# Performance work log

Measured on AMD Instinct MI355X. Metric: run time of the kernel, lower is better.

## Reference

```python
import jax, jax.numpy as jnp
import numpy as np

NF, NS, GP = 5, 27, 4


def conv2d(x, w, b):
    y = jax.lax.conv_general_dilated(x, w, (1, 1), 'SAME',
                                     dimension_numbers=('NCHW', 'OIHW', 'NCHW'))
    return y + b[None, :, None, None]


def trilinear_sample(frames, tc, yc, xc):
    # frames: [b, nf, h, w]; tc/yc/xc: [b, NS, h, w] absolute (t, y, x) coords
    b, nf, h, w = frames.shape
    tc = jnp.clip(tc, 0.0, nf - 1.0)
    yc = jnp.clip(yc, 0.0, h - 1.0)
    xc = jnp.clip(xc, 0.0, w - 1.0)
    t0 = jnp.floor(tc); y0 = jnp.floor(yc); x0 = jnp.floor(xc)
    wt = tc - t0; wy = yc - y0; wx = xc - x0
    t0i = t0.astype(jnp.int32); y0i = y0.astype(jnp.int32); x0i = x0.astype(jnp.int32)
    t1i = jnp.minimum(t0i + 1, nf - 1)
    y1i = jnp.minimum(y0i + 1, h - 1)
    x1i = jnp.minimum(x0i + 1, w - 1)
    flat = frames.reshape(b, -1)

    def g(ti, yi, xi):
        idx = (ti * h + yi) * w + xi  # [b, NS, h, w]
        return jnp.take_along_axis(flat, idx.reshape(b, -1), axis=1).reshape(idx.shape)

    c000 = g(t0i, y0i, x0i); c001 = g(t0i, y0i, x1i)
    c010 = g(t0i, y1i, x0i); c011 = g(t0i, y1i, x1i)
    c100 = g(t1i, y0i, x0i); c101 = g(t1i, y0i, x1i)
    c110 = g(t1i, y1i, x0i); c111 = g(t1i, y1i, x1i)
    c00 = c000 * (1 - wx) + c001 * wx
    c01 = c010 * (1 - wx) + c011 * wx
    c10 = c100 * (1 - wx) + c101 * wx
    c11 = c110 * (1 - wx) + c111 * wx
    c0 = c00 * (1 - wy) + c01 * wy
    c1 = c10 * (1 - wy) + c11 * wy
    return c0 * (1 - wt) + c1 * wt


def samp(frames, offset):
    # offset: [b, NS*3, h, w] -> per-sample (dt, dy, dx)
    b, nf, h, w = frames.shape
    off = offset.reshape(b, NS, 3, h, w)
    grid = np.stack(np.meshgrid(np.arange(-1, 2), np.arange(-1, 2), np.arange(-1, 2),
                                indexing='ij'), -1).reshape(NS, 3).astype(np.float32)
    bt = jnp.asarray(grid[:, 0] + (NF - 1) // 2)[None, :, None, None]
    by = jnp.asarray(grid[:, 1])[None, :, None, None]
    bx = jnp.asarray(grid[:, 2])[None, :, None, None]
    yy = jnp.arange(h, dtype=frames.dtype)[None, None, :, None]
    xx = jnp.arange(w, dtype=frames.dtype)[None, None, None, :]
    tc = off[:, :, 0] + bt
    yc = off[:, :, 1] + by + yy
    xc = off[:, :, 2] + bx + xx
    return trilinear_sample(frames, tc, yc, xc)  # [b, NS, h, w]


def reference(frames, ow1, ob1, ow2, ob2, ow3, ob3, ww1, wb1, ww2, wb2, ww3, wb3):
    b, c, h, w = frames.shape
    # OffsetNet: two relu convs -> feat (128 ch), head -> offsets (NS*3 ch)
    f1 = jax.nn.relu(conv2d(frames, ow1, ob1))
    feat = jax.nn.relu(conv2d(f1, ow2, ob2))
    offset = conv2d(feat, ow3, ob3)
    samples = samp(frames, offset)  # [b, 27, h, w]
    cat = jnp.concatenate([frames, feat, samples], axis=1)  # [b, 160, h, w]
    # WeightsNet: three conv+relu
    wgt = jax.nn.relu(conv2d(cat, ww1, wb1))
    wgt = jax.nn.relu(conv2d(wgt, ww2, wb2))
    wgt = jax.nn.relu(conv2d(wgt, ww3, wb3))  # [b, 27, h, w]
    npg = NS // GP  # 6 -> only first GP*npg=24 samples used (torch.split + range(gp))
    s = samples[:, :GP * npg].reshape(b, GP, npg, h, w)
    wg = wgt[:, :GP * npg].reshape(b, GP, npg, h, w)
    gp_pred = GP * jnp.sum(s * wg, axis=2)  # [b, 4, h, w]
    avg = jnp.sum(gp_pred, axis=1, keepdims=True) / NS
    return gp_pred, avg


def setup_inputs() -> dict:
    key = jax.random.key(0)
    ks = jax.random.split(key, 8)
    B, H, W = 4, 512, 512

    def he(k, shape):
        fan_in = shape[1] * shape[2] * shape[3]
        return jax.random.normal(k, shape, jnp.float32) * np.sqrt(2.0 / fan_in)

    return {
        'frames': jax.random.uniform(ks[0], (B, NF, H, W), jnp.float32),
        'ow1': he(ks[1], (64, NF, 3, 3)), 'ob1': jnp.zeros((64,), jnp.float32),
        'ow2': he(ks[2], (128, 64, 3, 3)), 'ob2': jnp.zeros((128,), jnp.float32),
        'ow3': he(ks[3], (NS * 3, 128, 3, 3)) * 0.1, 'ob3': jnp.zeros((NS * 3,), jnp.float32),
        'ww1': he(ks[4], (64, NF + 128 + NS, 3, 3)), 'wb1': jnp.zeros((64,), jnp.float32),
        'ww2': he(ks[5], (64, 64, 3, 3)), 'wb2': jnp.zeros((64,), jnp.float32),
        'ww3': he(ks[6], (NS, 64, 3, 3)), 'wb3': jnp.zeros((NS,), jnp.float32),
    }
```

## Files before the change

kernel.cpp:

```cpp
#include <hip/hip_runtime.h>

#define HH 512
#define WW 512
#define HWP (HH * WW)

typedef unsigned short bf16_t;
typedef short bf16x8 __attribute__((ext_vector_type(8)));
typedef float f32x4 __attribute__((ext_vector_type(4)));
typedef unsigned short us4 __attribute__((ext_vector_type(4)));
typedef unsigned short us8 __attribute__((ext_vector_type(8)));

__device__ __forceinline__ float bf2f(bf16_t h) {
    union { unsigned int u; float f; } v; v.u = ((unsigned int)h) << 16; return v.f;
}
__device__ __forceinline__ bf16_t f2bf(float f) {
    union { float f; unsigned int u; } v; v.f = f;
    unsigned int r = (v.u + 0x7FFFu + ((v.u >> 16) & 1u)) >> 16;
    return (bf16_t)r;
}
__device__ __forceinline__ bf16x8 as_bf(us8 v) {
    union { us8 a; bf16x8 b; } u; u.a = v; return u.b;
}
__device__ __forceinline__ void gload16(const void* g, void* l) {
    __builtin_amdgcn_global_load_lds(
        (const __attribute__((address_space(1))) void*)g,
        (__attribute__((address_space(3))) void*)l, 16, 0, 0);
}

__global__ __launch_bounds__(256) void wprep_all(
    const float* __restrict__ w1, const float* __restrict__ w2,
    const float* __restrict__ w3, const float* __restrict__ w4,
    const float* __restrict__ w5, const float* __restrict__ w6,
    bf16_t* __restrict__ dst)
{
    int i = blockIdx.x * 256 + threadIdx.x;
    if (i >= 350720) return;
    if (i >= 350208) { dst[i] = 0; return; }
    const float* w; int Cout, Cin, COTF, KS, perm, base;
    if (i < 18432)       { w = w1; base = 0;      Cout = 64;  Cin = 5;   COTF = 4; KS = 1; perm = 0; }
    else if (i < 92160)  { w = w2; base = 18432;  Cout = 128; Cin = 64;  COTF = 8; KS = 2; perm = 0; }
    else if (i < 202752) { w = w3; base = 92160;  Cout = 81;  Cin = 128; COTF = 6; KS = 4; perm = 0; }
    else if (i < 294912) { w = w4; base = 202752; Cout = 64;  Cin = 160; COTF = 4; KS = 5; perm = 1; }
    else if (i < 331776) { w = w5; base = 294912; Cout = 64;  Cin = 64;  COTF = 4; KS = 2; perm = 0; }
    else                 { w = w6; base = 331776; Cout = 27;  Cin = 64;  COTF = 2; KS = 2; perm = 0; }
    int r = i - base;
    int j = r & 7;
    int lane = (r >> 3) & 63;
    int cot = (r >> 9) % COTF;
    int rest = r / (512 * COTF);
    int ks = rest % KS, tap = rest / KS;
    int col = lane & 15, hi = lane >> 4;
    int co = cot * 16 + col;
    int ci = ks * 32 + hi * 8 + j;
    float v = 0.f;
    if (co < Cout && ci < Cin) {
        int rci = ci;
        if (perm) rci = (ci < 128) ? ci + 5 : (ci < 133 ? ci - 128 : ci);
        v = w[((size_t)co * Cin + rci) * 9 + tap];
    }
    dst[i] = f2bf(v);
}

template<int COT, int KS>
__global__ __launch_bounds__(256, 2) void tconv(
    const bf16_t* __restrict__ in, size_t inImgStride,
    const bf16_t* __restrict__ wt, const float* __restrict__ bias,
    bf16_t* __restrict__ out, size_t outImgStride,
    int COTF, int Cout, int relu, const bf16_t* __restrict__ zp)
{
    __shared__ us8 buf[2][1584];
    const int tid = threadIdx.x;
    const int wave = tid >> 6, lane = tid & 63;
    const int col = lane & 15, hi = lane >> 4;
    const int img = blockIdx.y >> 7;
    const int yb0 = (blockIdx.y & 127) * 4;
    const int xb = blockIdx.x * 64;
    const int czbase = blockIdx.z * COT;
    const size_t slab = (size_t)HH * WW * 32;

    in += (size_t)img * inImgStride;
    out += (size_t)img * outImgStride;

    int gofs[7];
    bool ok[7];
#pragma unroll
    for (int k = 0; k < 7; ++k) {
        int u = tid + k * 256;
        if (u >= 1584) u = 1583;
        int row = (unsigned)u / 264u;
        int rem = u - row * 264;
        int px = rem >> 2, cs = rem & 3;
        int c = (cs - (px >> 1)) & 3;
        int yin = yb0 - 1 + row;
        int gx = xb - 1 + px;
        ok[k] = ((unsigned)yin < (unsigned)HH) && ((unsigned)gx < (unsigned)WW);
        gofs[k] = ok[k] ? (int)(((size_t)yin * WW + gx) * 32 + c * 8) : 0;
    }

    auto STAGE = [&](int nb, int ks) {
#pragma unroll
        for (int k = 0; k < 7; ++k) {
            if (k == 6 && tid >= 48) continue;
            const bf16_t* g = ok[k] ? in + (size_t)ks * slab + gofs[k] : zp;
            gload16(g, (void*)&buf[nb][k * 256 + wave * 64]);
        }
    };

    f32x4 acc[4][COT] = {};
    bf16x8 a[9][COT];

    auto ALOAD = [&](int ks) {
#pragma unroll
        for (int t = 0; t < 9; ++t) {
#pragma unroll
            for (int c = 0; c < COT; ++c)
                a[t][c] = *(const bf16x8*)(wt
                    + (((size_t)t * KS + ks) * COTF + czbase + c) * 512 + lane * 8);
        }
    };

    auto COMPUTE = [&](int cb) {
#pragma unroll
        for (int dy = 0; dy < 3; ++dy) {
#pragma unroll
            for (int dx = 0; dx < 3; ++dx) {
                bf16x8 b[4];
#pragma unroll
                for (int pt = 0; pt < 4; ++pt) {
                    int X = pt * 16 + col + dx;
                    int unit = (wave + dy) * 264 + X * 4 + ((hi + (X >> 1)) & 3);
                    b[pt] = as_bf(buf[cb][unit]);
                }
#pragma unroll
                for (int c = 0; c < COT; ++c) {
#pragma unroll
                    for (int pt = 0; pt < 4; ++pt)
                        acc[pt][c] = __builtin_amdgcn_mfma_f32_16x16x32_bf16(
                            a[dy * 3 + dx][c], b[pt], acc[pt][c], 0, 0, 0);
                }
            }
        }
    };

    STAGE(0, 0);
    for (int ks = 0; ks < KS; ++ks) {
        ALOAD(ks);
        __builtin_amdgcn_sched_barrier(0);
        if (ks + 1 < KS) {
            STAGE((ks + 1) & 1, ks + 1);
            __builtin_amdgcn_sched_barrier(0);
            asm volatile("s_waitcnt vmcnt(7)" ::: "memory");
        } else {
            asm volatile("s_waitcnt vmcnt(0)" ::: "memory");
        }
        __builtin_amdgcn_sched_barrier(0);
        __builtin_amdgcn_s_barrier();
        __builtin_amdgcn_sched_barrier(0);
        COMPUTE(ks & 1);
        __builtin_amdgcn_s_barrier();
        __builtin_amdgcn_sched_barrier(0);
    }

    int y = yb0 + wave;
#pragma unroll
    for (int c = 0; c < COT; ++c) {
        int chbase = (czbase + c) * 16 + hi * 4;
        int slice = chbase >> 5, rem = chbase & 31;
        float bv[4];
#pragma unroll
        for (int j = 0; j < 4; ++j) {
            int co = chbase + j;
            bv[j] = (co < Cout) ? bias[co] : 0.f;
        }
#pragma unroll
        for (int pt = 0; pt < 4; ++pt) {
            int x = xb + pt * 16 + col;
            us4 o;
#pragma unroll
            for (int j = 0; j < 4; ++j) {
                float v = acc[pt][c][j] + bv[j];
                if (relu) v = fmaxf(v, 0.f);
                o[j] = f2bf(v);
            }
            *(us4*)(out + (((size_t)slice * HH + y) * WW + x) * 32 + rem) = o;
        }
    }
}

__global__ __launch_bounds__(256) void tr_fr32(
    const float* __restrict__ fr0, int img0,
    bf16_t* __restrict__ dst0, size_t stride)
{
    int img = blockIdx.y;
    int i = blockIdx.x * 256 + threadIdx.x;
    const float* fr = fr0 + (size_t)(img0 + img) * 5 * HWP;
    bf16_t* dst = dst0 + (size_t)img * stride;
    us8 v0 = {};
#pragma unroll
    for (int c = 0; c < 5; ++c) v0[c] = f2bf(fr[(size_t)c * HWP + i]);
    us8 z = {};
    us8* o = (us8*)(dst + (size_t)i * 32);
    o[0] = v0; o[1] = z; o[2] = z; o[3] = z;
}

__global__ __launch_bounds__(256, 4) void sample27f(
    const float* __restrict__ fr0, int img0,
    const bf16_t* __restrict__ of0, size_t stride,
    bf16_t* __restrict__ cat0)
{
    int img = blockIdx.y;
    int i = blockIdx.x * 256 + threadIdx.x;
    int y = i >> 9, x = i & 511;
    const float* f = fr0 + (size_t)(img0 + img) * 5 * HWP;
    const bf16_t* off = of0 + (size_t)img * stride;
    bf16_t* cat = cat0 + (size_t)img * stride;

    us8 ov[12];
#pragma unroll
    for (int sl = 0; sl < 3; ++sl)
#pragma unroll
        for (int c = 0; c < 4; ++c)
            ov[sl * 4 + c] = *(const us8*)(off
                + (((size_t)sl * HH + y) * WW + x) * 32 + c * 8);

    us8 outv[4];
#pragma unroll
    for (int c = 0; c < 5; ++c)
        outv[0][c] = f2bf(f[(size_t)c * HWP + i]);

#pragma unroll
    for (int s = 0; s < 27; ++s) {
        float dt  = bf2f((bf16_t)ov[(3 * s) >> 3][(3 * s) & 7]);
        float dyo = bf2f((bf16_t)ov[(3 * s + 1) >> 3][(3 * s + 1) & 7]);
        float dxo = bf2f((bf16_t)ov[(3 * s + 2) >> 3][(3 * s + 2) & 7]);
        float tc = dt + (float)(s / 9 + 1);
        float yc = dyo + (float)((s / 3) % 3 - 1) + (float)y;
        float xc = dxo + (float)(s % 3 - 1) + (float)x;
        tc = fminf(fmaxf(tc, 0.f), 4.f);
        yc = fminf(fmaxf(yc, 0.f), 511.f);
        xc = fminf(fmaxf(xc, 0.f), 511.f);
        float t0f = floorf(tc), y0f = floorf(yc), x0f = floorf(xc);
        float wt = tc - t0f, wy = yc - y0f, wx = xc - x0f;
        int t0 = (int)t0f, y0 = (int)y0f, x0 = (int)x0f;
        int t1 = min(t0 + 1, 4), y1 = min(y0 + 1, 511), x1 = min(x0 + 1, 511);
        float c000 = f[((size_t)t0 * HH + y0) * WW + x0];
        float c001 = f[((size_t)t0 * HH + y0) * WW + x1];
        float c010 = f[((size_t)t0 * HH + y1) * WW + x0];
        float c011 = f[((size_t)t0 * HH + y1) * WW + x1];
        float c100 = f[((size_t)t1 * HH + y0) * WW + x0];
        float c101 = f[((size_t)t1 * HH + y0) * WW + x1];
        float c110 = f[((size_t)t1 * HH + y1) * WW + x0];
        float c111 = f[((size_t)t1 * HH + y1) * WW + x1];
        float c00 = c000 * (1.f - wx) + c001 * wx;
        float c01 = c010 * (1.f - wx) + c011 * wx;
        float c10 = c100 * (1.f - wx) + c101 * wx;
        float c11 = c110 * (1.f - wx) + c111 * wx;
        float c0 = c00 * (1.f - wy) + c01 * wy;
        float c1 = c10 * (1.f - wy) + c11 * wy;
        int ch = 5 + s;
        outv[ch >> 3][ch & 7] = f2bf(c0 * (1.f - wt) + c1 * wt);
    }

    us8* o = (us8*)(cat + ((size_t)y * WW + x) * 32);
    o[0] = outv[0]; o[1] = outv[1]; o[2] = outv[2]; o[3] = outv[3];
}

__global__ __launch_bounds__(256) void combineN(
    const bf16_t* __restrict__ cat0, const bf16_t* __restrict__ wg0,
    size_t stride, float* __restrict__ out, int img0)
{
    int img = blockIdx.y;
    int i = blockIdx.x * 256 + threadIdx.x;
    int gimg = img0 + img;
    const bf16_t* sp = cat0 + (size_t)img * stride + (size_t)i * 32 + 5;
    const bf16_t* wp = wg0 + (size_t)img * stride + (size_t)i * 32;
    float* ogp  = out + (size_t)gimg * 4 * HWP;
    float* oavg = out + (size_t)16 * HWP + (size_t)gimg * HWP;
    float total = 0.f;
#pragma unroll
    for (int g = 0; g < 4; ++g) {
        float acc = 0.f;
#pragma unroll
        for (int j = 0; j < 6; ++j)
            acc += bf2f(sp[g * 6 + j]) * bf2f(wp[g * 6 + j]);
        float gp = 4.f * acc;
        ogp[(size_t)g * HWP + i] = gp;
        total += gp;
    }
    oavg[i] = total / 27.f;
}

static inline int cdiv(int a, int b) { return (a + b - 1) / b; }

extern "C" void kernel_launch(void* const* d_in, const int* in_sizes, int n_in,
                              void* d_out, int out_size, void* d_ws, size_t ws_size,
                              hipStream_t stream)
{
    const float* frames = (const float*)d_in[0];
    const float* ow1 = (const float*)d_in[1];
    const float* ob1 = (const float*)d_in[2];
    const float* ow2 = (const float*)d_in[3];
    const float* ob2 = (const float*)d_in[4];
    const float* ow3 = (const float*)d_in[5];
    const float* ob3 = (const float*)d_in[6];
    const float* ww1 = (const float*)d_in[7];
    const float* wb1 = (const float*)d_in[8];
    const float* ww2 = (const float*)d_in[9];
    const float* wb2 = (const float*)d_in[10];
    const float* ww3 = (const float*)d_in[11];
    const float* wb3 = (const float*)d_in[12];
    float* out = (float*)d_out;

    bf16_t* Wp = (bf16_t*)d_ws;
    const size_t wo1 = 0;
    const size_t wo2 = 18432;
    const size_t wo3 = 92160;
    const size_t wo4 = 202752;
    const size_t wo5 = 294912;
    const size_t wo6 = 331776;
    const size_t wzp = 350208;
    const size_t wtot = 350720;

    const size_t SLAB = (size_t)HH * WW * 32;
    const size_t PerImg = 7 * SLAB;

    size_t availElems = ws_size / sizeof(bf16_t);
    int NB = 1;
    if (wtot + 4 * PerImg <= availElems) NB = 4;
    else if (wtot + 2 * PerImg <= availElems) NB = 2;

    bf16_t* ZP = Wp + wzp;
    bf16_t* WS = Wp + wtot;

    wprep_all<<<cdiv(350720, 256), 256, 0, stream>>>(ow1, ow2, ow3, ww1, ww2, ww3, Wp);

    for (int s = 0; s < 4; s += NB) {
        int nb = (4 - s < NB) ? (4 - s) : NB;
        bf16_t* S0 = WS;
        bf16_t* S2 = WS + 2 * SLAB;
        bf16_t* S4 = WS + 4 * SLAB;
        bf16_t* S5 = WS + 5 * SLAB;
        bf16_t* S6 = WS + 6 * SLAB;

        tr_fr32<<<dim3(1024, nb), 256, 0, stream>>>(frames, s, S6, PerImg);
        tconv<4, 1><<<dim3(8, 128 * nb, 1), 256, 0, stream>>>(
            S6, PerImg, Wp + wo1, ob1, S4, PerImg, 4, 64, 1, ZP);
        tconv<4, 2><<<dim3(8, 128 * nb, 2), 256, 0, stream>>>(
            S4, PerImg, Wp + wo2, ob2, S0, PerImg, 8, 128, 1, ZP);
        tconv<3, 4><<<dim3(8, 128 * nb, 2), 256, 0, stream>>>(
            S0, PerImg, Wp + wo3, ob3, S4, PerImg, 6, 81, 0, ZP);
        sample27f<<<dim3(1024, nb), 256, 0, stream>>>(frames, s, S4, PerImg, S4);
        tconv<4, 5><<<dim3(8, 128 * nb, 1), 256, 0, stream>>>(
            S0, PerImg, Wp + wo4, wb1, S5, PerImg, 4, 64, 1, ZP);
        tconv<4, 2><<<dim3(8, 128 * nb, 1), 256, 0, stream>>>(
            S5, PerImg, Wp + wo5, wb2, S0, PerImg, 4, 64, 1, ZP);
        tconv<2, 2><<<dim3(8, 128 * nb, 1), 256, 0, stream>>>(
            S0, PerImg, Wp + wo6, wb3, S2, PerImg, 2, 27, 1, ZP);
        combineN<<<dim3(1024, nb), 256, 0, stream>>>(S4, S2, PerImg, out, s);
    }
}
```

Baseline: 1.026 ms.

## Fuse weighted combine into final conv epilogue, skip zero-channel loads

Removes the separate combineN kernel by computing the grouped weighted sums and average directly from the last conv's accumulators, using cross-lane shuffles to reduce over channels. The first conv now loads zeros instead of reading padded channels beyond cinCh, so tr_fr32 no longer writes the zero padding. The vmcnt wait counts are also changed per COT, presumably to account for A-operand loads issued alongside the staging. This removes one full-image write and read of the weight tensor. The cost is a more complex epilogue in the conv kernel, and the hand-picked wait counts could be wrong.

```diff
diff --git a/kernel.cpp b/kernel.cpp
--- a/kernel.cpp
+++ b/kernel.cpp
@@ -66,7 +66,9 @@
     const bf16_t* __restrict__ in, size_t inImgStride,
     const bf16_t* __restrict__ wt, const float* __restrict__ bias,
     bf16_t* __restrict__ out, size_t outImgStride,
-    int COTF, int Cout, int relu, const bf16_t* __restrict__ zp)
+    int COTF, int Cout, int relu, const bf16_t* __restrict__ zp,
+    int cinCh, const bf16_t* __restrict__ catp,
+    float* __restrict__ fuseOut, int img0)
 {
     __shared__ us8 buf[2][1584];
     const int tid = threadIdx.x;
@@ -93,7 +95,8 @@
         int c = (cs - (px >> 1)) & 3;
         int yin = yb0 - 1 + row;
         int gx = xb - 1 + px;
-        ok[k] = ((unsigned)yin < (unsigned)HH) && ((unsigned)gx < (unsigned)WW);
+        ok[k] = ((unsigned)yin < (unsigned)HH) && ((unsigned)gx < (unsigned)WW)
+                && (c < cinCh);
         gofs[k] = ok[k] ? (int)(((size_t)yin * WW + gx) * 32 + c * 8) : 0;
     }
 
@@ -149,9 +152,19 @@
         if (ks + 1 < KS) {
             STAGE((ks + 1) & 1, ks + 1);
             __builtin_amdgcn_sched_barrier(0);
-            asm volatile("s_waitcnt vmcnt(7)" ::: "memory");
+            if constexpr (COT == 4)
+                asm volatile("s_waitcnt vmcnt(42)" ::: "memory");
+            else if constexpr (COT == 3)
+                asm volatile("s_waitcnt vmcnt(33)" ::: "memory");
+            else
+                asm volatile("s_waitcnt vmcnt(24)" ::: "memory");
         } else {
-            asm volatile("s_waitcnt vmcnt(0)" ::: "memory");
+            if constexpr (COT == 4)
+                asm volatile("s_waitcnt vmcnt(36)" ::: "memory");
+            else if constexpr (COT == 3)
+                asm volatile("s_waitcnt vmcnt(27)" ::: "memory");
+            else
+                asm volatile("s_waitcnt vmcnt(18)" ::: "memory");
         }
         __builtin_amdgcn_sched_barrier(0);
         __builtin_amdgcn_s_barrier();
@@ -162,6 +175,47 @@
     }
 
     int y = yb0 + wave;
+
+    if (fuseOut) {
+        int gimg = img0 + img;
+        const bf16_t* catim = catp + (size_t)img * inImgStride;
+#pragma unroll
+        for (int pt = 0; pt < 4; ++pt) {
+            int x = xb + pt * 16 + col;
+            const bf16_t* cp = catim + ((size_t)y * WW + x) * 32;
+            float p[4] = {0.f, 0.f, 0.f, 0.f};
+#pragma unroll
+            for (int c = 0; c < COT; ++c) {
+                int chb = (czbase + c) * 16 + hi * 4;
+#pragma unroll
+                for (int j = 0; j < 4; ++j) {
+                    int ch = chb + j;
+                    if (ch < 24) {
+                        float wv = fmaxf(acc[pt][c][j] + bias[ch], 0.f);
+                        p[ch / 6] += wv * bf2f(cp[5 + ch]);
+                    }
+                }
+            }
+#pragma unroll
+            for (int g = 0; g < 4; ++g) {
+                p[g] += __shfl_xor(p[g], 16);
+                p[g] += __shfl_xor(p[g], 32);
+            }
+            if (hi == 0) {
+                size_t pix = (size_t)y * WW + x;
+                float tot = 0.f;
+#pragma unroll
+                for (int g = 0; g < 4; ++g) {
+                    float gp = 4.f * p[g];
+                    fuseOut[((size_t)gimg * 4 + g) * HWP + pix] = gp;
+                    tot += gp;
+                }
+                fuseOut[(size_t)16 * HWP + (size_t)gimg * HWP + pix] = tot / 27.f;
+            }
+        }
+        return;
+    }
+
 #pragma unroll
     for (int c = 0; c < COT; ++c) {
         int chbase = (czbase + c) * 16 + hi * 4;
@@ -198,9 +252,7 @@
     us8 v0 = {};
 #pragma unroll
     for (int c = 0; c < 5; ++c) v0[c] = f2bf(fr[(size_t)c * HWP + i]);
-    us8 z = {};
-    us8* o = (us8*)(dst + (size_t)i * 32);
-    o[0] = v0; o[1] = z; o[2] = z; o[3] = z;
+    *(us8*)(dst + (size_t)i * 32) = v0;
 }
 
 __global__ __launch_bounds__(256, 4) void sample27f(
@@ -265,31 +317,6 @@
     o[0] = outv[0]; o[1] = outv[1]; o[2] = outv[2]; o[3] = outv[3];
 }
 
-__global__ __launch_bounds__(256) void combineN(
-    const bf16_t* __restrict__ cat0, const bf16_t* __restrict__ wg0,
-    size_t stride, float* __restrict__ out, int img0)
-{
-    int img = blockIdx.y;
-    int i = blockIdx.x * 256 + threadIdx.x;
-    int gimg = img0 + img;
-    const bf16_t* sp = cat0 + (size_t)img * stride + (size_t)i * 32 + 5;
-    const bf16_t* wp = wg0 + (size_t)img * stride + (size_t)i * 32;
-    float* ogp  = out + (size_t)gimg * 4 * HWP;
-    float* oavg = out + (size_t)16 * HWP + (size_t)gimg * HWP;
-    float total = 0.f;
-#pragma unroll
-    for (int g = 0; g < 4; ++g) {
-        float acc = 0.f;
-#pragma unroll
-        for (int j = 0; j < 6; ++j)
-            acc += bf2f(sp[g * 6 + j]) * bf2f(wp[g * 6 + j]);
-        float gp = 4.f * acc;
-        ogp[(size_t)g * HWP + i] = gp;
-        total += gp;
-    }
-    oavg[i] = total / 27.f;
-}
-
 static inline int cdiv(int a, int b) { return (a + b - 1) / b; }
 
 extern "C" void kernel_launch(void* const* d_in, const int* in_sizes, int n_in,
@@ -344,18 +371,23 @@
 
         tr_fr32<<<dim3(1024, nb), 256, 0, stream>>>(frames, s, S6, PerImg);
         tconv<4, 1><<<dim3(8, 128 * nb, 1), 256, 0, stream>>>(
-            S6, PerImg, Wp + wo1, ob1, S4, PerImg, 4, 64, 1, ZP);
+            S6, PerImg, Wp + wo1, ob1, S4, PerImg, 4, 64, 1, ZP,
+            1, nullptr, nullptr, 0);
         tconv<4, 2><<<dim3(8, 128 * nb, 2), 256, 0, stream>>>(
-            S4, PerImg, Wp + wo2, ob2, S0, PerImg, 8, 128, 1, ZP);
+            S4, PerImg, Wp + wo2, ob2, S0, PerImg, 8, 128, 1, ZP,
+            4, nullptr, nullptr, 0);
         tconv<3, 4><<<dim3(8, 128 * nb, 2), 256, 0, stream>>>(
-            S0, PerImg, Wp + wo3, ob3, S4, PerImg, 6, 81, 0, ZP);
+            S0, PerImg, Wp + wo3, ob3, S4, PerImg, 6, 81, 0, ZP,
+            4, nullptr, nullptr, 0);
         sample27f<<<dim3(1024, nb), 256, 0, stream>>>(frames, s, S4, PerImg, S4);
         tconv<4, 5><<<dim3(8, 128 * nb, 1), 256, 0, stream>>>(
-            S0, PerImg, Wp + wo4, wb1, S5, PerImg, 4, 64, 1, ZP);
+            S0, PerImg, Wp + wo4, wb1, S5, PerImg, 4, 64, 1, ZP,
+            4, nullptr, nullptr, 0);
         tconv<4, 2><<<dim3(8, 128 * nb, 1), 256, 0, stream>>>(
-            S5, PerImg, Wp + wo5, wb2, S0, PerImg, 4, 64, 1, ZP);
+            S5, PerImg, Wp + wo5, wb2, S0, PerImg, 4, 64, 1, ZP,
+            4, nullptr, nullptr, 0);
         tconv<2, 2><<<dim3(8, 128 * nb, 1), 256, 0, stream>>>(
-            S0, PerImg, Wp + wo6, wb3, S2, PerImg, 2, 27, 1, ZP);
-        combineN<<<dim3(1024, nb), 256, 0, stream>>>(S4, S2, PerImg, out, s);
-    }
-}
+            S0, PerImg, Wp + wo6, wb3, S2, PerImg, 2, 27, 1, ZP,
+            4, S4, out, s);
+    }
+}
```

New measurement: 1.035 ms. About the same (+0.8%).
